# Kernel optimization log

Hardware: AMD Instinct MI355X
Metric: run time of the kernel (lower is better)

The kernel has to match this reference:

```python
import jax, jax.numpy as jnp
import numpy as np

N_NODES = 100000
N_EDGES = 3200000
N_FEAT = 128
DIM = 256
N_CLASSES = 16
BN_EPS = 1e-5


def _glorot(key, shape):
    fan_in, fan_out = shape[0], shape[1]
    lim = float(np.sqrt(6.0 / (fan_in + fan_out)))
    return jax.random.uniform(key, shape, jnp.float32, -lim, lim)


def setup_inputs() -> dict:
    key = jax.random.key(0)
    ks = jax.random.split(key, 16)
    x = jax.random.normal(ks[0], (N_NODES, N_FEAT), jnp.float32)
    edge_index = jax.random.randint(ks[1], (2, N_EDGES), 0, N_NODES, jnp.int64)
    inp = {"x": x, "edge_index": edge_index}
    # conv1 MLP: num_features -> dim -> dim
    inp["w1a"] = _glorot(ks[2], (N_FEAT, DIM)); inp["b1a"] = jnp.zeros((DIM,), jnp.float32)
    inp["w1b"] = _glorot(ks[3], (DIM, DIM));    inp["b1b"] = jnp.zeros((DIM,), jnp.float32)
    inp["g1"] = jnp.ones((DIM,), jnp.float32);  inp["be1"] = jnp.zeros((DIM,), jnp.float32)
    # conv2 MLP
    inp["w2a"] = _glorot(ks[4], (DIM, DIM)); inp["b2a"] = jnp.zeros((DIM,), jnp.float32)
    inp["w2b"] = _glorot(ks[5], (DIM, DIM)); inp["b2b"] = jnp.zeros((DIM,), jnp.float32)
    inp["g2"] = jnp.ones((DIM,), jnp.float32); inp["be2"] = jnp.zeros((DIM,), jnp.float32)
    # conv3 MLP
    inp["w3a"] = _glorot(ks[6], (DIM, DIM)); inp["b3a"] = jnp.zeros((DIM,), jnp.float32)
    inp["w3b"] = _glorot(ks[7], (DIM, DIM)); inp["b3b"] = jnp.zeros((DIM,), jnp.float32)
    # fc2: dim -> num_classes
    inp["wfc"] = _glorot(ks[8], (DIM, N_CLASSES)); inp["bfc"] = jnp.zeros((N_CLASSES,), jnp.float32)
    return inp


def _gin_conv(h, src, dst, wa, ba, wb, bb):
    # sum-aggregate neighbor features: agg[i] = sum_{(j->i)} h[j]; eps=0 so root weight = 1
    agg = jax.ops.segment_sum(h[src], dst, num_segments=N_NODES)
    z = jax.nn.relu((h + agg) @ wa + ba)
    return z @ wb + bb


def _batchnorm(h, gamma, beta):
    # training-mode BN over node dim (biased variance, as torch forward)
    m = h.mean(axis=0)
    v = ((h - m) ** 2).mean(axis=0)
    return gamma * (h - m) / jnp.sqrt(v + BN_EPS) + beta


def reference(x, edge_index, w1a, b1a, w1b, b1b, g1, be1,
              w2a, b2a, w2b, b2b, g2, be2,
              w3a, b3a, w3b, b3b, wfc, bfc):
    src, dst = edge_index[0], edge_index[1]
    h = jax.nn.relu(_gin_conv(x, src, dst, w1a, b1a, w1b, b1b))
    h = _batchnorm(h, g1, be1)
    h = jax.nn.relu(_gin_conv(h, src, dst, w2a, b2a, w2b, b2b))
    h = _batchnorm(h, g2, be2)
    h = jax.nn.relu(_gin_conv(h, src, dst, w3a, b3a, w3b, b3b))
    # dropout p=0.5 is identity in eval mode
    logits = h @ wfc + bfc
    return jax.nn.log_softmax(logits, axis=-1)
```

## Files before the change

kernel.cpp:

```cpp
#include <hip/hip_runtime.h>

typedef unsigned int  u32;
typedef unsigned short u16;

#define NND 100000
#define MPAD 100096
#define NE  3200000
#define F0  128
#define DIM 256
#define NC  16

#define BSH   9
#define NBUCK 196
#define CAP   18432
#define EPB   8192

typedef __bf16 bf16x8 __attribute__((ext_vector_type(8)));
typedef float  f32x4  __attribute__((ext_vector_type(4)));

__device__ __forceinline__ float b2f(u16 h){ return __uint_as_float(((u32)h)<<16); }
__device__ __forceinline__ u16 f2b(float f){
    u32 u = __float_as_uint(f);
    return (u16)((u + 0x7fffu + ((u>>16)&1u)) >> 16);
}
__device__ __forceinline__ float lo16(u32 u){ return __uint_as_float(u<<16); }
__device__ __forceinline__ float hi16(u32 u){ return __uint_as_float(u & 0xffff0000u); }

__device__ __forceinline__ void gload16(const u16* g, u16* l){
    __builtin_amdgcn_global_load_lds(
        (const __attribute__((address_space(1))) u32*)g,
        (__attribute__((address_space(3))) u32*)l, 16, 0, 0);
}

__global__ void probe_kernel(const u32* __restrict__ xw, const int* __restrict__ ei,
                             int* __restrict__ mode){
    if(threadIdx.x==0 && blockIdx.x==0){
        int insane = 0;
        for(int i=0;i<64;i++){
            u32 w  = xw[i];
            u32 lo = w & 0xffffu;
            u32 e  = (lo >> 7) & 0xff;
            if(lo != 0 && (e < 48 || e > 208)) insane++;
        }
        mode[0] = (insane > 8) ? 1 : 0;
        int zeros = 0;
        for(int i=0;i<16;i++) if(ei[2*i+1]==0) zeros++;
        mode[1] = (zeros==16) ? 1 : 0;
    }
}

__device__ __forceinline__ int ld_src(const int* ei, int i64f, long e){
    return i64f ? ei[2*e] : ei[e];
}
__device__ __forceinline__ int ld_dst(const int* ei, int i64f, long e){
    return i64f ? ei[2*((long)NE + e)] : ei[(long)NE + e];
}

__global__ __launch_bounds__(256) void bucketA(const int* __restrict__ ei,
        const int* __restrict__ mode, u32* __restrict__ bucketArr,
        int* __restrict__ gcur){
    __shared__ u32 stag[EPB];
    __shared__ u16 sbuck[EPB];
    __shared__ int cnt[NBUCK];
    __shared__ int ofs[NBUCK];
    __shared__ int wofs[NBUCK];
    __shared__ int gbase[NBUCK];
    __shared__ int ps[256];
    int tid = threadIdx.x;
    int i64f = mode[1];
    long e0 = (long)blockIdx.x * EPB;
    int n = (int)min((long)EPB, (long)NE - e0);
    if(tid < NBUCK) cnt[tid] = 0;
    __syncthreads();
    for(int i=tid;i<n;i+=256){
        int d = ld_dst(ei, i64f, e0+i);
        atomicAdd(&cnt[d>>BSH], 1);
    }
    __syncthreads();
    ps[tid] = (tid < NBUCK) ? cnt[tid] : 0;
    __syncthreads();
    for(int o=1;o<256;o<<=1){
        int v = (tid>=o) ? ps[tid-o] : 0;
        __syncthreads();
        ps[tid] += v;
        __syncthreads();
    }
    if(tid < NBUCK){
        int ex = ps[tid] - cnt[tid];
        ofs[tid] = ex; wofs[tid] = ex;
        gbase[tid] = cnt[tid] ? atomicAdd(&gcur[tid], cnt[tid]) : 0;
    }
    __syncthreads();
    for(int i=tid;i<n;i+=256){
        int s = ld_src(ei, i64f, e0+i);
        int d = ld_dst(ei, i64f, e0+i);
        int b = d>>BSH;
        int r = atomicAdd(&wofs[b], 1);
        stag[r]  = ((u32)s<<BSH) | (u32)(d & ((1<<BSH)-1));
        sbuck[r] = (u16)b;
    }
    __syncthreads();
    for(int i=tid;i<n;i+=256){
        int b = sbuck[i];
        int pos = gbase[b] + (i - ofs[b]);
        if(pos < CAP) bucketArr[(size_t)b*CAP + pos] = stag[i];
    }
}

__global__ void scan_buckets(const int* __restrict__ gcur, int* __restrict__ bbase){
    __shared__ int ps[256];
    int t = threadIdx.x;
    int c = (t < NBUCK) ? gcur[t] : 0;
    ps[t] = c;
    __syncthreads();
    for(int o=1;o<256;o<<=1){
        int v = (t>=o) ? ps[t-o] : 0;
        __syncthreads();
        ps[t] += v;
        __syncthreads();
    }
    if(t < NBUCK) bbase[t] = ps[t] - c;
}

__global__ __launch_bounds__(256) void bucketB(const u32* __restrict__ bucketArr,
        const int* __restrict__ gcnt, const int* __restrict__ bbase,
        int* __restrict__ rp, int* __restrict__ ssrc){
    __shared__ u32 stag[CAP];
    __shared__ int deg[512];
    __shared__ int lrp[512];
    __shared__ int cur[512];
    __shared__ int ps[256];
    int b = blockIdx.x, tid = threadIdx.x;
    int n = min(gcnt[b], CAP);
    int base = bbase[b];
    const u32* ba = bucketArr + (size_t)b*CAP;
    deg[tid] = 0; deg[tid+256] = 0;
    __syncthreads();
    for(int i=tid;i<n;i+=256){
        atomicAdd(&deg[ba[i] & 511], 1);
    }
    __syncthreads();
    ps[tid] = deg[2*tid] + deg[2*tid+1];
    __syncthreads();
    for(int o=1;o<256;o<<=1){
        int v = (tid>=o) ? ps[tid-o] : 0;
        __syncthreads();
        ps[tid] += v;
        __syncthreads();
    }
    {
        int ep = (tid==0) ? 0 : ps[tid-1];
        lrp[2*tid]   = ep;
        lrp[2*tid+1] = ep + deg[2*tid];
        cur[2*tid]   = lrp[2*tid];
        cur[2*tid+1] = lrp[2*tid+1];
    }
    __syncthreads();
    for(int i=tid;i<512;i+=256){
        int node = (b<<BSH) + i;
        if(node <= NND) rp[node] = base + lrp[i];
    }
    for(int i=tid;i<n;i+=256){
        u32 v = ba[i];
        int r = atomicAdd(&cur[v & 511], 1);
        stag[r] = v >> BSH;
    }
    __syncthreads();
    for(int i=tid;i<n;i+=256){
        ssrc[base + i] = (int)stag[i];
    }
}

__global__ void cvt_x(const float* __restrict__ xf, u16* __restrict__ Xc,
                      const int* __restrict__ mode){
    if(!mode[0]) return;
    size_t i = ((size_t)blockIdx.x*256 + threadIdx.x)*8;
    float4 a = *(const float4*)(xf+i);
    float4 b = *(const float4*)(xf+i+4);
    uint4 pk;
    pk.x = (u32)f2b(a.x) | ((u32)f2b(a.y)<<16);
    pk.y = (u32)f2b(a.z) | ((u32)f2b(a.w)<<16);
    pk.z = (u32)f2b(b.x) | ((u32)f2b(b.y)<<16);
    pk.w = (u32)f2b(b.z) | ((u32)f2b(b.w)<<16);
    *(uint4*)(Xc + i) = pk;
}

__global__ void transpose_cvt(const void* __restrict__ W, u16* __restrict__ Wt,
                              int K, int N, const int* __restrict__ mode){
    int id = blockIdx.x*256 + threadIdx.x;
    if(id < K*N){
        int k = id / N, n = id % N;
        float v = mode[0] ? ((const float*)W)[id] : b2f(((const u16*)W)[id]);
        Wt[n*K + k] = f2b(v);
    }
}

__global__ void cvt_wfc(const void* __restrict__ W, u16* __restrict__ Wc,
                        const int* __restrict__ mode){
    int id = blockIdx.x*256 + threadIdx.x;
    int k = id / NC, c = id % NC;
    float v = mode[0] ? ((const float*)W)[id] : b2f(((const u16*)W)[id]);
    Wc[c*DIM + k] = f2b(v);
}

__global__ void cvt_vecs(const void* p0, const void* p1, const void* p2, const void* p3,
                         const void* p4, const void* p5, const void* p6, const void* p7,
                         const void* p8, const void* p9, const void* p10,
                         u16* __restrict__ Vc, const int* __restrict__ mode){
    const void* ps[11] = {p0,p1,p2,p3,p4,p5,p6,p7,p8,p9,p10};
    int lens[11] = {DIM,DIM,DIM,DIM,DIM,DIM,DIM,DIM,DIM,DIM,NC};
    int b = blockIdx.x, t = threadIdx.x;
    if(t < lens[b]){
        float v = mode[0] ? ((const float*)ps[b])[t] : b2f(((const u16*)ps[b])[t]);
        Vc[b*256 + t] = f2b(v);
    }
}

template<int VEC>
__global__ __launch_bounds__(256) void agg_kernel(const u16* __restrict__ hA,
        const u16* __restrict__ hB, const int* __restrict__ mode,
        const int* __restrict__ rp, const int* __restrict__ ssrc,
        u16* __restrict__ out,
        const float* __restrict__ stats, const u16* __restrict__ g,
        const u16* __restrict__ be, int use_bn, int M){
    const int F = 64*VEC;
    int node = blockIdx.x*4 + (threadIdx.x>>6);
    if(node >= M) return;
    int lane = threadIdx.x & 63;
    int lv = lane*VEC;
    const u16* h = (VEC==2 && mode[0]) ? hB : hA;

    float acc[VEC];
    {
        const u16* bp = h + (size_t)node*F + lv;
        if(VEC==4){
            uint2 u = *(const uint2*)bp;
            acc[0]=lo16(u.x); acc[1]=hi16(u.x); acc[2]=lo16(u.y); acc[3]=hi16(u.y);
        } else {
            u32 u = *(const u32*)bp;
            acc[0]=lo16(u); acc[1]=hi16(u);
        }
    }

    auto gather4 = [&](int s0,int s1,int s2,int s3){
        const u16* p0 = h + (size_t)s0*F + lv;
        const u16* p1 = h + (size_t)s1*F + lv;
        const u16* p2 = h + (size_t)s2*F + lv;
        const u16* p3 = h + (size_t)s3*F + lv;
        if(VEC==4){
            uint2 u0=*(const uint2*)p0, u1=*(const uint2*)p1,
                  u2=*(const uint2*)p2, u3=*(const uint2*)p3;
            acc[0]+=lo16(u0.x)+lo16(u1.x)+lo16(u2.x)+lo16(u3.x);
            acc[1]+=hi16(u0.x)+hi16(u1.x)+hi16(u2.x)+hi16(u3.x);
            acc[2]+=lo16(u0.y)+lo16(u1.y)+lo16(u2.y)+lo16(u3.y);
            acc[3]+=hi16(u0.y)+hi16(u1.y)+hi16(u2.y)+hi16(u3.y);
        } else {
            u32 u0=*(const u32*)p0, u1=*(const u32*)p1,
                u2=*(const u32*)p2, u3=*(const u32*)p3;
            acc[0]+=lo16(u0)+lo16(u1)+lo16(u2)+lo16(u3);
            acc[1]+=hi16(u0)+hi16(u1)+hi16(u2)+hi16(u3);
        }
    };

    int e0 = rp[node], e1 = rp[node+1];
    int e = e0;
    int eend = e0 + ((e1-e0) & ~3);
    if(e < eend){
        int s0=ssrc[e+0], s1=ssrc[e+1], s2=ssrc[e+2], s3=ssrc[e+3];
        e += 4;
        for(; e < eend; e += 4){
            int t0=ssrc[e+0], t1=ssrc[e+1], t2=ssrc[e+2], t3=ssrc[e+3];
            gather4(s0,s1,s2,s3);
            s0=t0; s1=t1; s2=t2; s3=t3;
        }
        gather4(s0,s1,s2,s3);
    }
    for(; e<e1; e++){
        int s = ssrc[e];
        const u16* sp = h + (size_t)s*F + lv;
        if(VEC==4){
            uint2 u = *(const uint2*)sp;
            acc[0]+=lo16(u.x); acc[1]+=hi16(u.x); acc[2]+=lo16(u.y); acc[3]+=hi16(u.y);
        } else {
            u32 u = *(const u32*)sp;
            acc[0]+=lo16(u); acc[1]+=hi16(u);
        }
    }

    float aff_a[VEC], aff_b[VEC];
    if(use_bn){
        float inv_m = 1.0f / (float)M;
        #pragma unroll
        for(int v=0; v<VEC; v++){
            int f = lv + v;
            float mean = stats[f]*inv_m;
            float var  = fmaxf(stats[F+f]*inv_m - mean*mean, 0.f);
            float rstd = rsqrtf(var + 1e-5f);
            float gg = b2f(g[f]);
            aff_a[v] = gg*rstd;
            aff_b[v] = b2f(be[f]) - gg*rstd*mean;
        }
    } else {
        #pragma unroll
        for(int v=0; v<VEC; v++){ aff_a[v]=1.f; aff_b[v]=0.f; }
    }
    float cnt = (float)(e1-e0+1);

    u16* op = out + (size_t)node*F + lv;
    if(VEC==4){
        uint2 o;
        float r0 = aff_a[0]*acc[0] + cnt*aff_b[0];
        float r1 = aff_a[1]*acc[1] + cnt*aff_b[1];
        float r2 = aff_a[2]*acc[2] + cnt*aff_b[2];
        float r3 = aff_a[3]*acc[3] + cnt*aff_b[3];
        o.x = (u32)f2b(r0) | ((u32)f2b(r1)<<16);
        o.y = (u32)f2b(r2) | ((u32)f2b(r3)<<16);
        *(uint2*)op = o;
    } else {
        float r0 = aff_a[0]*acc[0] + cnt*aff_b[0];
        float r1 = aff_a[1]*acc[1] + cnt*aff_b[1];
        *(u32*)op = (u32)f2b(r0) | ((u32)f2b(r1)<<16);
    }
}

#define TBM 128
#define TBN 128
#define TBK 32
__global__ __launch_bounds__(256) void gemm128(
        const u16* __restrict__ A, const u16* __restrict__ Bt,
        const u16* __restrict__ bias, u16* __restrict__ C,
        int N, int K, int do_relu, float* __restrict__ stats, int do_stats){
    __shared__ __align__(16) u16 lA[TBM*TBK];
    __shared__ __align__(16) u16 lB[TBN*TBK];
    __shared__ float colS[TBN], colS2[TBN];
    int tid = threadIdx.x;
    int w = tid>>6, lane = tid&63;
    int q = lane>>4, mr = lane&15;
    int wr = w>>1, wc = w&1;
    int m0 = blockIdx.x*TBM, n0 = blockIdx.y*TBN;

    if(do_stats){
        if(tid < TBN){ colS[tid]=0.f; colS2[tid]=0.f; }
    }

    f32x4 acc[4][4];
    #pragma unroll
    for(int i=0;i<4;i++)
        #pragma unroll
        for(int c=0;c<4;c++) acc[i][c] = (f32x4){0.f,0.f,0.f,0.f};

    const u16* ga0 = A  + (size_t)(m0 + w*32 + (lane>>2))*K + (lane&3)*8;
    const u16* ga1 = ga0 + (size_t)16*K;
    const u16* gb0 = Bt + (size_t)(n0 + w*32 + (lane>>2))*K + (lane&3)*8;
    const u16* gb1 = gb0 + (size_t)16*K;
    u16* la0 = &lA[(w*32)*TBK];    u16* la1 = la0 + 16*TBK;
    u16* lb0 = &lB[(w*32)*TBK];    u16* lb1 = lb0 + 16*TBK;

    for(int k0=0; k0<K; k0+=TBK){
        gload16(ga0, la0); gload16(ga1, la1);
        gload16(gb0, lb0); gload16(gb1, lb1);
        ga0 += TBK; ga1 += TBK; gb0 += TBK; gb1 += TBK;
        __syncthreads();
        bf16x8 af[4], bfr[4];
        #pragma unroll
        for(int i=0;i<4;i++)
            af[i] = *reinterpret_cast<const bf16x8*>(&lA[(wr*64 + i*16 + mr)*TBK + q*8]);
        #pragma unroll
        for(int c=0;c<4;c++)
            bfr[c] = *reinterpret_cast<const bf16x8*>(&lB[(wc*64 + c*16 + mr)*TBK + q*8]);
        #pragma unroll
        for(int i=0;i<4;i++)
            #pragma unroll
            for(int c=0;c<4;c++)
                acc[i][c] = __builtin_amdgcn_mfma_f32_16x16x32_bf16(af[i], bfr[c], acc[i][c], 0, 0, 0);
        __syncthreads();
    }

    #pragma unroll
    for(int c=0;c<4;c++){
        int lcol = wc*64 + c*16 + mr;
        int col  = n0 + lcol;
        float bv = b2f(bias[col]);
        float s = 0.f, s2 = 0.f;
        #pragma unroll
        for(int i=0;i<4;i++){
            int row = m0 + wr*64 + i*16 + q*4;
            #pragma unroll
            for(int r=0;r<4;r++){
                float v = acc[i][c][r] + bv;
                if(do_relu) v = fmaxf(v, 0.f);
                u16 o = f2b(v);
                C[(size_t)(row + r)*N + col] = o;
                if(do_stats && (row + r) < NND){
                    float vr = b2f(o);
                    s += vr; s2 += vr*vr;
                }
            }
        }
        if(do_stats){
            atomicAdd(&colS[lcol], s);
            atomicAdd(&colS2[lcol], s2);
        }
    }
    if(do_stats){
        __syncthreads();
        if(tid < TBN){
            int col = n0 + tid;
            atomicAdd(&stats[col], colS[tid]);
            atomicAdd(&stats[DIM+col], colS2[tid]);
        }
    }
}

__global__ __launch_bounds__(256) void fc_lsm(const u16* __restrict__ h,
        const u16* __restrict__ wfcT, const u16* __restrict__ bfc,
        void* __restrict__ out, const int* __restrict__ mode, int M){
    __shared__ float lds[256];
    __shared__ float rmx[16], rls[16];
    int tid = threadIdx.x;
    int r = tid>>4, c = tid&15;
    int row = blockIdx.x*16 + r;
    float acc = b2f(bfc[c]);
    const u16* hp = h + (size_t)row*DIM;
    const u16* wp = wfcT + c*DIM;
    for(int k=0;k<DIM;k+=8){
        uint4 hv = *(const uint4*)(hp+k);
        uint4 wv = *(const uint4*)(wp+k);
        acc += lo16(hv.x)*lo16(wv.x) + hi16(hv.x)*hi16(wv.x)
             + lo16(hv.y)*lo16(wv.y) + hi16(hv.y)*hi16(wv.y)
             + lo16(hv.z)*lo16(wv.z) + hi16(hv.z)*hi16(wv.z)
             + lo16(hv.w)*lo16(wv.w) + hi16(hv.w)*hi16(wv.w);
    }
    lds[tid] = acc;
    __syncthreads();
    if(c==0){
        float mx = -1e30f;
        for(int i=0;i<NC;i++) mx = fmaxf(mx, lds[r*NC+i]);
        float s = 0.f;
        for(int i=0;i<NC;i++) s += expf(lds[r*NC+i] - mx);
        rmx[r] = mx; rls[r] = logf(s);
    }
    __syncthreads();
    if(row < M){
        float v = acc - rmx[r] - rls[r];
        if(mode[0]) ((float*)out)[(size_t)row*NC + c] = v;
        else        ((u16*)out)[(size_t)row*NC + c] = f2b(v);
    }
}

extern "C" void kernel_launch(void* const* d_in, const int* in_sizes, int n_in,
                              void* d_out, int out_size, void* d_ws, size_t ws_size,
                              hipStream_t stream){
    const void* x   = d_in[0];
    const int*  ei  = (const int*)d_in[1];
    const void* w1a = d_in[2];  const void* b1a = d_in[3];
    const void* w1b = d_in[4];  const void* b1b = d_in[5];
    const void* g1  = d_in[6];  const void* be1 = d_in[7];
    const void* w2a = d_in[8];  const void* b2a = d_in[9];
    const void* w2b = d_in[10]; const void* b2b = d_in[11];
    const void* g2  = d_in[12]; const void* be2 = d_in[13];
    const void* w3a = d_in[14]; const void* b3a = d_in[15];
    const void* w3b = d_in[16]; const void* b3b = d_in[17];
    const void* wfc = d_in[18]; const void* bfc = d_in[19];

    char* base = (char*)d_ws;
    size_t off = 0;
    auto alloc = [&](size_t bytes)->void*{
        void* p = base + off;
        off = (off + bytes + 255) & ~(size_t)255;
        return p;
    };
    u16*  P     = (u16*)alloc((size_t)MPAD*DIM*2);
    u16*  Q     = (u16*)alloc((size_t)MPAD*DIM*2);
    int*  ssrc  = (int*)alloc((size_t)NE*4);
    u32*  bArr  = (u32*)alloc((size_t)NBUCK*CAP*4);
    int*  gcur  = (int*)alloc((size_t)NBUCK*4);
    int*  bbase = (int*)alloc((size_t)NBUCK*4);
    int*  rp    = (int*)alloc((size_t)(NND+1)*4);
    float* stats= (float*)alloc(2*DIM*4);
    int*  mode  = (int*)alloc(16);
    u16* Wt1a = (u16*)alloc((size_t)F0*DIM*2);
    u16* Wt1b = (u16*)alloc((size_t)DIM*DIM*2);
    u16* Wt2a = (u16*)alloc((size_t)DIM*DIM*2);
    u16* Wt2b = (u16*)alloc((size_t)DIM*DIM*2);
    u16* Wt3a = (u16*)alloc((size_t)DIM*DIM*2);
    u16* Wt3b = (u16*)alloc((size_t)DIM*DIM*2);
    u16* Vc   = (u16*)alloc(11*256*2);
    u16* Wfc  = (u16*)alloc((size_t)DIM*NC*2);
    u16* Xc   = P;

    probe_kernel<<<1, 64, 0, stream>>>((const u32*)x, ei, mode);

    hipMemsetAsync(gcur, 0, (size_t)NBUCK*4, stream);
    bucketA<<<(NE + EPB - 1)/EPB, 256, 0, stream>>>(ei, mode, bArr, gcur);
    scan_buckets<<<1, 256, 0, stream>>>(gcur, bbase);
    bucketB<<<NBUCK, 256, 0, stream>>>(bArr, gcur, bbase, rp, ssrc);

    cvt_x<<<(NND*F0)/(256*8), 256, 0, stream>>>((const float*)x, Xc, mode);
    transpose_cvt<<<(F0*DIM+255)/256, 256, 0, stream>>>(w1a, Wt1a, F0, DIM, mode);
    transpose_cvt<<<(DIM*DIM+255)/256, 256, 0, stream>>>(w1b, Wt1b, DIM, DIM, mode);
    transpose_cvt<<<(DIM*DIM+255)/256, 256, 0, stream>>>(w2a, Wt2a, DIM, DIM, mode);
    transpose_cvt<<<(DIM*DIM+255)/256, 256, 0, stream>>>(w2b, Wt2b, DIM, DIM, mode);
    transpose_cvt<<<(DIM*DIM+255)/256, 256, 0, stream>>>(w3a, Wt3a, DIM, DIM, mode);
    transpose_cvt<<<(DIM*DIM+255)/256, 256, 0, stream>>>(w3b, Wt3b, DIM, DIM, mode);
    cvt_wfc<<<(DIM*NC)/256, 256, 0, stream>>>(wfc, Wfc, mode);
    cvt_vecs<<<11, 256, 0, stream>>>(b1a,b1b,g1,be1,b2a,b2b,g2,be2,b3a,b3b,bfc, Vc, mode);

    dim3 ggrid(MPAD/TBM, DIM/TBN);

    hipMemsetAsync(stats, 0, 2*DIM*4, stream);
    agg_kernel<2><<<NND/4, 256, 0, stream>>>((const u16*)x, Xc, mode, rp, ssrc, Q,
                                             stats, Vc, Vc, 0, NND);
    gemm128<<<ggrid, 256, 0, stream>>>(Q, Wt1a, Vc+0*256, P, DIM, F0, 1, stats, 0);
    gemm128<<<ggrid, 256, 0, stream>>>(P, Wt1b, Vc+1*256, Q, DIM, DIM, 1, stats, 1);

    agg_kernel<4><<<NND/4, 256, 0, stream>>>(Q, Q, mode, rp, ssrc, P,
                                             stats, Vc+2*256, Vc+3*256, 1, NND);
    hipMemsetAsync(stats, 0, 2*DIM*4, stream);
    gemm128<<<ggrid, 256, 0, stream>>>(P, Wt2a, Vc+4*256, Q, DIM, DIM, 1, stats, 0);
    gemm128<<<ggrid, 256, 0, stream>>>(Q, Wt2b, Vc+5*256, P, DIM, DIM, 1, stats, 1);

    agg_kernel<4><<<NND/4, 256, 0, stream>>>(P, P, mode, rp, ssrc, Q,
                                             stats, Vc+6*256, Vc+7*256, 1, NND);
    gemm128<<<ggrid, 256, 0, stream>>>(Q, Wt3a, Vc+8*256, P, DIM, DIM, 1, stats, 0);
    gemm128<<<ggrid, 256, 0, stream>>>(P, Wt3b, Vc+9*256, Q, DIM, DIM, 1, stats, 0);

    fc_lsm<<<NND/16, 256, 0, stream>>>(Q, Wfc, Vc+10*256, d_out, mode, NND);
}
```

Before: 1.178 ms.

## Rewrite neighbor aggregation to 16-byte gathers across edge slots, merge setup kernels

The aggregation kernel now has each lane load 8 bf16 features (16 bytes) and splits a wavefront across several edges at once, combining the partial sums with cross-lane shuffles. Before, each lane loaded 2 or 4 features and all 64 lanes walked the same edge list in sequence. The goal is wider memory transactions and more gathers in flight per node. Separately, the weight and vector conversion kernels are merged into one launch, the bucket prefix scan moves into bucketB, and the memsets are folded into the probe kernel using double-buffered stats, which cuts launch count. The costs are that every bucketB block repeats the scan, and shuffle reductions are added per node.

After: 1.153 ms. 1.02x faster.

```diff
diff --git a/kernel.cpp b/kernel.cpp
--- a/kernel.cpp
+++ b/kernel.cpp
@@ -33,8 +33,13 @@
 }
 
 __global__ void probe_kernel(const u32* __restrict__ xw, const int* __restrict__ ei,
-                             int* __restrict__ mode){
-    if(threadIdx.x==0 && blockIdx.x==0){
+                             int* __restrict__ mode, int* __restrict__ gcur,
+                             float* __restrict__ stats){
+    int t = threadIdx.x;
+    if(t < NBUCK) gcur[t] = 0;
+    #pragma unroll
+    for(int i=0;i<4;i++) stats[t + 256*i] = 0.f;
+    if(t==0){
         int insane = 0;
         for(int i=0;i<64;i++){
             u32 w  = xw[i];
@@ -107,23 +112,8 @@
     }
 }
 
-__global__ void scan_buckets(const int* __restrict__ gcur, int* __restrict__ bbase){
-    __shared__ int ps[256];
-    int t = threadIdx.x;
-    int c = (t < NBUCK) ? gcur[t] : 0;
-    ps[t] = c;
-    __syncthreads();
-    for(int o=1;o<256;o<<=1){
-        int v = (t>=o) ? ps[t-o] : 0;
-        __syncthreads();
-        ps[t] += v;
-        __syncthreads();
-    }
-    if(t < NBUCK) bbase[t] = ps[t] - c;
-}
-
 __global__ __launch_bounds__(256) void bucketB(const u32* __restrict__ bucketArr,
-        const int* __restrict__ gcnt, const int* __restrict__ bbase,
+        const int* __restrict__ gcnt,
         int* __restrict__ rp, int* __restrict__ ssrc){
     __shared__ u32 stag[CAP];
     __shared__ int deg[512];
@@ -131,8 +121,16 @@
     __shared__ int cur[512];
     __shared__ int ps[256];
     int b = blockIdx.x, tid = threadIdx.x;
+    ps[tid] = (tid < NBUCK) ? gcnt[tid] : 0;
+    __syncthreads();
+    for(int o=1;o<256;o<<=1){
+        int v = (tid>=o) ? ps[tid-o] : 0;
+        __syncthreads();
+        ps[tid] += v;
+        __syncthreads();
+    }
+    int base = (b>0) ? ps[b-1] : 0;
     int n = min(gcnt[b], CAP);
-    int base = bbase[b];
     const u32* ba = bucketArr + (size_t)b*CAP;
     deg[tid] = 0; deg[tid+256] = 0;
     __syncthreads();
@@ -185,141 +183,136 @@
     *(uint4*)(Xc + i) = pk;
 }
 
-__global__ void transpose_cvt(const void* __restrict__ W, u16* __restrict__ Wt,
-                              int K, int N, const int* __restrict__ mode){
-    int id = blockIdx.x*256 + threadIdx.x;
-    if(id < K*N){
-        int k = id / N, n = id % N;
-        float v = mode[0] ? ((const float*)W)[id] : b2f(((const u16*)W)[id]);
-        Wt[n*K + k] = f2b(v);
-    }
-}
-
-__global__ void cvt_wfc(const void* __restrict__ W, u16* __restrict__ Wc,
-                        const int* __restrict__ mode){
-    int id = blockIdx.x*256 + threadIdx.x;
-    int k = id / NC, c = id % NC;
-    float v = mode[0] ? ((const float*)W)[id] : b2f(((const u16*)W)[id]);
-    Wc[c*DIM + k] = f2b(v);
-}
-
-__global__ void cvt_vecs(const void* p0, const void* p1, const void* p2, const void* p3,
-                         const void* p4, const void* p5, const void* p6, const void* p7,
-                         const void* p8, const void* p9, const void* p10,
-                         u16* __restrict__ Vc, const int* __restrict__ mode){
-    const void* ps[11] = {p0,p1,p2,p3,p4,p5,p6,p7,p8,p9,p10};
-    int lens[11] = {DIM,DIM,DIM,DIM,DIM,DIM,DIM,DIM,DIM,DIM,NC};
+__device__ __forceinline__ float ldf(const void* p, int i, int f32f){
+    return f32f ? ((const float*)p)[i] : b2f(((const u16*)p)[i]);
+}
+__global__ void merged_cvt(
+        const void* w1a, const void* w1b, const void* w2a, const void* w2b,
+        const void* w3a, const void* w3b, const void* wfc,
+        const void* b1a, const void* b1b, const void* g1, const void* be1,
+        const void* b2a, const void* b2b, const void* g2, const void* be2,
+        const void* b3a, const void* b3b, const void* bfcp,
+        u16* __restrict__ Wt1a, u16* __restrict__ Wt1b, u16* __restrict__ Wt2a,
+        u16* __restrict__ Wt2b, u16* __restrict__ Wt3a, u16* __restrict__ Wt3b,
+        u16* __restrict__ Wfc, u16* __restrict__ Vc, const int* __restrict__ mode){
     int b = blockIdx.x, t = threadIdx.x;
-    if(t < lens[b]){
-        float v = mode[0] ? ((const float*)ps[b])[t] : b2f(((const u16*)ps[b])[t]);
-        Vc[b*256 + t] = f2b(v);
-    }
-}
-
-template<int VEC>
-__global__ __launch_bounds__(256) void agg_kernel(const u16* __restrict__ hA,
+    int f32f = mode[0];
+    if(b < 128){
+        int id = b*256 + t;
+        int k = id / DIM, n = id % DIM;
+        Wt1a[n*F0 + k] = f2b(ldf(w1a, id, f32f));
+        return;
+    }
+    b -= 128;
+    if(b < 5*256){
+        int wi = b >> 8;
+        const void* W = (wi==0)?w1b:(wi==1)?w2a:(wi==2)?w2b:(wi==3)?w3a:w3b;
+        u16* Wt = (wi==0)?Wt1b:(wi==1)?Wt2a:(wi==2)?Wt2b:(wi==3)?Wt3a:Wt3b;
+        int id = (b & 255)*256 + t;
+        int k = id / DIM, n = id % DIM;
+        Wt[n*DIM + k] = f2b(ldf(W, id, f32f));
+        return;
+    }
+    b -= 5*256;
+    if(b < 16){
+        int id = b*256 + t;
+        int k = id / NC, c = id % NC;
+        Wfc[c*DIM + k] = f2b(ldf(wfc, id, f32f));
+        return;
+    }
+    b -= 16;
+    {
+        const void* ps[11] = {b1a,b1b,g1,be1,b2a,b2b,g2,be2,b3a,b3b,bfcp};
+        int lens[11] = {DIM,DIM,DIM,DIM,DIM,DIM,DIM,DIM,DIM,DIM,NC};
+        if(t < lens[b]) Vc[b*256 + t] = f2b(ldf(ps[b], t, f32f));
+    }
+}
+
+template<int LPI>
+__global__ __launch_bounds__(256) void agg2(const u16* __restrict__ hA,
         const u16* __restrict__ hB, const int* __restrict__ mode,
         const int* __restrict__ rp, const int* __restrict__ ssrc,
         u16* __restrict__ out,
         const float* __restrict__ stats, const u16* __restrict__ g,
         const u16* __restrict__ be, int use_bn, int M){
-    const int F = 64*VEC;
+    const int F = LPI*8;
+    const int IPW = 64/LPI;
     int node = blockIdx.x*4 + (threadIdx.x>>6);
     if(node >= M) return;
     int lane = threadIdx.x & 63;
-    int lv = lane*VEC;
-    const u16* h = (VEC==2 && mode[0]) ? hB : hA;
-
-    float acc[VEC];
-    {
-        const u16* bp = h + (size_t)node*F + lv;
-        if(VEC==4){
-            uint2 u = *(const uint2*)bp;
-            acc[0]=lo16(u.x); acc[1]=hi16(u.x); acc[2]=lo16(u.y); acc[3]=hi16(u.y);
+    int li   = lane & (LPI-1);
+    int slot = lane / LPI;
+    const u16* h = (LPI==16 && mode[0]) ? hB : hA;
+    const int boff = li*8;
+
+    int e0 = rp[node], e1 = rp[node+1];
+    int n_items = e1 - e0 + 1;
+    float acc[8] = {0.f,0.f,0.f,0.f,0.f,0.f,0.f,0.f};
+
+    auto item = [&](int i)->int { return (i==0) ? node : ssrc[e0 + i - 1]; };
+    auto addu = [&](uint4 u){
+        acc[0]+=lo16(u.x); acc[1]+=hi16(u.x);
+        acc[2]+=lo16(u.y); acc[3]+=hi16(u.y);
+        acc[4]+=lo16(u.z); acc[5]+=hi16(u.z);
+        acc[6]+=lo16(u.w); acc[7]+=hi16(u.w);
+    };
+
+    int i = 0;
+    for(; i + 4*IPW <= n_items; i += 4*IPW){
+        int s0 = item(i + slot);
+        int s1 = item(i + IPW + slot);
+        int s2 = item(i + 2*IPW + slot);
+        int s3 = item(i + 3*IPW + slot);
+        uint4 u0 = *(const uint4*)(h + (size_t)s0*F + boff);
+        uint4 u1 = *(const uint4*)(h + (size_t)s1*F + boff);
+        uint4 u2 = *(const uint4*)(h + (size_t)s2*F + boff);
+        uint4 u3 = *(const uint4*)(h + (size_t)s3*F + boff);
+        addu(u0); addu(u1); addu(u2); addu(u3);
+    }
+    for(; i + IPW <= n_items; i += IPW){
+        int s = item(i + slot);
+        addu(*(const uint4*)(h + (size_t)s*F + boff));
+    }
+    if(i < n_items){
+        int r = n_items - i;
+        if(slot < r){
+            int s = item(i + slot);
+            addu(*(const uint4*)(h + (size_t)s*F + boff));
+        }
+    }
+
+    #pragma unroll
+    for(int j=0;j<8;j++){
+        if(LPI==16) acc[j] += __shfl_xor(acc[j], 16);
+        acc[j] += __shfl_xor(acc[j], 32);
+    }
+
+    if(slot == 0){
+        float res[8];
+        if(use_bn){
+            float inv_m = 1.0f / (float)M;
+            float cnt = (float)n_items;
+            #pragma unroll
+            for(int j=0;j<8;j++){
+                int f = boff + j;
+                float mean = stats[f]*inv_m;
+                float var  = fmaxf(stats[F+f]*inv_m - mean*mean, 0.f);
+                float rstd = rsqrtf(var + 1e-5f);
+                float gg = b2f(g[f]);
+                float a = gg*rstd;
+                float bb = b2f(be[f]) - a*mean;
+                res[j] = a*acc[j] + cnt*bb;
+            }
         } else {
-            u32 u = *(const u32*)bp;
-            acc[0]=lo16(u); acc[1]=hi16(u);
+            #pragma unroll
+            for(int j=0;j<8;j++) res[j] = acc[j];
         }
-    }
-
-    auto gather4 = [&](int s0,int s1,int s2,int s3){
-        const u16* p0 = h + (size_t)s0*F + lv;
-        const u16* p1 = h + (size_t)s1*F + lv;
-        const u16* p2 = h + (size_t)s2*F + lv;
-        const u16* p3 = h + (size_t)s3*F + lv;
-        if(VEC==4){
-            uint2 u0=*(const uint2*)p0, u1=*(const uint2*)p1,
-                  u2=*(const uint2*)p2, u3=*(const uint2*)p3;
-            acc[0]+=lo16(u0.x)+lo16(u1.x)+lo16(u2.x)+lo16(u3.x);
-            acc[1]+=hi16(u0.x)+hi16(u1.x)+hi16(u2.x)+hi16(u3.x);
-            acc[2]+=lo16(u0.y)+lo16(u1.y)+lo16(u2.y)+lo16(u3.y);
-            acc[3]+=hi16(u0.y)+hi16(u1.y)+hi16(u2.y)+hi16(u3.y);
-        } else {
-            u32 u0=*(const u32*)p0, u1=*(const u32*)p1,
-                u2=*(const u32*)p2, u3=*(const u32*)p3;
-            acc[0]+=lo16(u0)+lo16(u1)+lo16(u2)+lo16(u3);
-            acc[1]+=hi16(u0)+hi16(u1)+hi16(u2)+hi16(u3);
-        }
-    };
-
-    int e0 = rp[node], e1 = rp[node+1];
-    int e = e0;
-    int eend = e0 + ((e1-e0) & ~3);
-    if(e < eend){
-        int s0=ssrc[e+0], s1=ssrc[e+1], s2=ssrc[e+2], s3=ssrc[e+3];
-        e += 4;
-        for(; e < eend; e += 4){
-            int t0=ssrc[e+0], t1=ssrc[e+1], t2=ssrc[e+2], t3=ssrc[e+3];
-            gather4(s0,s1,s2,s3);
-            s0=t0; s1=t1; s2=t2; s3=t3;
-        }
-        gather4(s0,s1,s2,s3);
-    }
-    for(; e<e1; e++){
-        int s = ssrc[e];
-        const u16* sp = h + (size_t)s*F + lv;
-        if(VEC==4){
-            uint2 u = *(const uint2*)sp;
-            acc[0]+=lo16(u.x); acc[1]+=hi16(u.x); acc[2]+=lo16(u.y); acc[3]+=hi16(u.y);
-        } else {
-            u32 u = *(const u32*)sp;
-            acc[0]+=lo16(u); acc[1]+=hi16(u);
-        }
-    }
-
-    float aff_a[VEC], aff_b[VEC];
-    if(use_bn){
-        float inv_m = 1.0f / (float)M;
-        #pragma unroll
-        for(int v=0; v<VEC; v++){
-            int f = lv + v;
-            float mean = stats[f]*inv_m;
-            float var  = fmaxf(stats[F+f]*inv_m - mean*mean, 0.f);
-            float rstd = rsqrtf(var + 1e-5f);
-            float gg = b2f(g[f]);
-            aff_a[v] = gg*rstd;
-            aff_b[v] = b2f(be[f]) - gg*rstd*mean;
-        }
-    } else {
-        #pragma unroll
-        for(int v=0; v<VEC; v++){ aff_a[v]=1.f; aff_b[v]=0.f; }
-    }
-    float cnt = (float)(e1-e0+1);
-
-    u16* op = out + (size_t)node*F + lv;
-    if(VEC==4){
-        uint2 o;
-        float r0 = aff_a[0]*acc[0] + cnt*aff_b[0];
-        float r1 = aff_a[1]*acc[1] + cnt*aff_b[1];
-        float r2 = aff_a[2]*acc[2] + cnt*aff_b[2];
-        float r3 = aff_a[3]*acc[3] + cnt*aff_b[3];
-        o.x = (u32)f2b(r0) | ((u32)f2b(r1)<<16);
-        o.y = (u32)f2b(r2) | ((u32)f2b(r3)<<16);
-        *(uint2*)op = o;
-    } else {
-        float r0 = aff_a[0]*acc[0] + cnt*aff_b[0];
-        float r1 = aff_a[1]*acc[1] + cnt*aff_b[1];
-        *(u32*)op = (u32)f2b(r0) | ((u32)f2b(r1)<<16);
+        uint4 o;
+        o.x = (u32)f2b(res[0]) | ((u32)f2b(res[1])<<16);
+        o.y = (u32)f2b(res[2]) | ((u32)f2b(res[3])<<16);
+        o.z = (u32)f2b(res[4]) | ((u32)f2b(res[5])<<16);
+        o.w = (u32)f2b(res[6]) | ((u32)f2b(res[7])<<16);
+        *(uint4*)(out + (size_t)node*F + boff) = o;
     }
 }
 
@@ -475,9 +468,8 @@
     int*  ssrc  = (int*)alloc((size_t)NE*4);
     u32*  bArr  = (u32*)alloc((size_t)NBUCK*CAP*4);
     int*  gcur  = (int*)alloc((size_t)NBUCK*4);
-    int*  bbase = (int*)alloc((size_t)NBUCK*4);
     int*  rp    = (int*)alloc((size_t)(NND+1)*4);
-    float* stats= (float*)alloc(2*DIM*4);
+    float* stats= (float*)alloc(4*DIM*4);
     int*  mode  = (int*)alloc(16);
     u16* Wt1a = (u16*)alloc((size_t)F0*DIM*2);
     u16* Wt1b = (u16*)alloc((size_t)DIM*DIM*2);
@@ -488,42 +480,35 @@
     u16* Vc   = (u16*)alloc(11*256*2);
     u16* Wfc  = (u16*)alloc((size_t)DIM*NC*2);
     u16* Xc   = P;
-
-    probe_kernel<<<1, 64, 0, stream>>>((const u32*)x, ei, mode);
-
-    hipMemsetAsync(gcur, 0, (size_t)NBUCK*4, stream);
+    float* statsA = stats;
+    float* statsB = stats + 2*DIM;
+
+    probe_kernel<<<1, 256, 0, stream>>>((const u32*)x, ei, mode, gcur, stats);
+
     bucketA<<<(NE + EPB - 1)/EPB, 256, 0, stream>>>(ei, mode, bArr, gcur);
-    scan_buckets<<<1, 256, 0, stream>>>(gcur, bbase);
-    bucketB<<<NBUCK, 256, 0, stream>>>(bArr, gcur, bbase, rp, ssrc);
+    bucketB<<<NBUCK, 256, 0, stream>>>(bArr, gcur, rp, ssrc);
 
     cvt_x<<<(NND*F0)/(256*8), 256, 0, stream>>>((const float*)x, Xc, mode);
-    transpose_cvt<<<(F0*DIM+255)/256, 256, 0, stream>>>(w1a, Wt1a, F0, DIM, mode);
-    transpose_cvt<<<(DIM*DIM+255)/256, 256, 0, stream>>>(w1b, Wt1b, DIM, DIM, mode);
-    transpose_cvt<<<(DIM*DIM+255)/256, 256, 0, stream>>>(w2a, Wt2a, DIM, DIM, mode);
-    transpose_cvt<<<(DIM*DIM+255)/256, 256, 0, stream>>>(w2b, Wt2b, DIM, DIM, mode);
-    transpose_cvt<<<(DIM*DIM+255)/256, 256, 0, stream>>>(w3a, Wt3a, DIM, DIM, mode);
-    transpose_cvt<<<(DIM*DIM+255)/256, 256, 0, stream>>>(w3b, Wt3b, DIM, DIM, mode);
-    cvt_wfc<<<(DIM*NC)/256, 256, 0, stream>>>(wfc, Wfc, mode);
-    cvt_vecs<<<11, 256, 0, stream>>>(b1a,b1b,g1,be1,b2a,b2b,g2,be2,b3a,b3b,bfc, Vc, mode);
+    merged_cvt<<<128 + 5*256 + 16 + 11, 256, 0, stream>>>(
+        w1a,w1b,w2a,w2b,w3a,w3b,wfc, b1a,b1b,g1,be1,b2a,b2b,g2,be2,b3a,b3b,bfc,
+        Wt1a,Wt1b,Wt2a,Wt2b,Wt3a,Wt3b,Wfc,Vc, mode);
 
     dim3 ggrid(MPAD/TBM, DIM/TBN);
 
-    hipMemsetAsync(stats, 0, 2*DIM*4, stream);
-    agg_kernel<2><<<NND/4, 256, 0, stream>>>((const u16*)x, Xc, mode, rp, ssrc, Q,
-                                             stats, Vc, Vc, 0, NND);
-    gemm128<<<ggrid, 256, 0, stream>>>(Q, Wt1a, Vc+0*256, P, DIM, F0, 1, stats, 0);
-    gemm128<<<ggrid, 256, 0, stream>>>(P, Wt1b, Vc+1*256, Q, DIM, DIM, 1, stats, 1);
-
-    agg_kernel<4><<<NND/4, 256, 0, stream>>>(Q, Q, mode, rp, ssrc, P,
-                                             stats, Vc+2*256, Vc+3*256, 1, NND);
-    hipMemsetAsync(stats, 0, 2*DIM*4, stream);
-    gemm128<<<ggrid, 256, 0, stream>>>(P, Wt2a, Vc+4*256, Q, DIM, DIM, 1, stats, 0);
-    gemm128<<<ggrid, 256, 0, stream>>>(Q, Wt2b, Vc+5*256, P, DIM, DIM, 1, stats, 1);
-
-    agg_kernel<4><<<NND/4, 256, 0, stream>>>(P, P, mode, rp, ssrc, Q,
-                                             stats, Vc+6*256, Vc+7*256, 1, NND);
-    gemm128<<<ggrid, 256, 0, stream>>>(Q, Wt3a, Vc+8*256, P, DIM, DIM, 1, stats, 0);
-    gemm128<<<ggrid, 256, 0, stream>>>(P, Wt3b, Vc+9*256, Q, DIM, DIM, 1, stats, 0);
+    agg2<16><<<NND/4, 256, 0, stream>>>((const u16*)x, Xc, mode, rp, ssrc, Q,
+                                        statsA, Vc, Vc, 0, NND);
+    gemm128<<<ggrid, 256, 0, stream>>>(Q, Wt1a, Vc+0*256, P, DIM, F0, 1, statsA, 0);
+    gemm128<<<ggrid, 256, 0, stream>>>(P, Wt1b, Vc+1*256, Q, DIM, DIM, 1, statsA, 1);
+
+    agg2<32><<<NND/4, 256, 0, stream>>>(Q, Q, mode, rp, ssrc, P,
+                                        statsA, Vc+2*256, Vc+3*256, 1, NND);
+    gemm128<<<ggrid, 256, 0, stream>>>(P, Wt2a, Vc+4*256, Q, DIM, DIM, 1, statsB, 0);
+    gemm128<<<ggrid, 256, 0, stream>>>(Q, Wt2b, Vc+5*256, P, DIM, DIM, 1, statsB, 1);
+
+    agg2<32><<<NND/4, 256, 0, stream>>>(P, P, mode, rp, ssrc, Q,
+                                        statsB, Vc+6*256, Vc+7*256, 1, NND);
+    gemm128<<<ggrid, 256, 0, stream>>>(Q, Wt3a, Vc+8*256, P, DIM, DIM, 1, statsA, 0);
+    gemm128<<<ggrid, 256, 0, stream>>>(P, Wt3b, Vc+9*256, Q, DIM, DIM, 1, statsA, 0);
 
     fc_lsm<<<NND/16, 256, 0, stream>>>(Q, Wfc, Vc+10*256, d_out, mode, NND);
 }
```
